# Kernel tuning notes

Hardware: AMD Instinct MI355X
Metric: run time of the kernel (lower is better)

## Reference

```python
import jax, jax.numpy as jnp
import numpy as np

M = 500000   # num_type_node_G1 (nodes in sub-graph G1_sub1)
D = 128      # embedding_dim
S = 0        # start_idx
E = 8000000  # number of nonzero adjacency entries (avg degree 16)


def setup_inputs() -> dict:
    key = jax.random.key(0)
    k1, k2 = jax.random.split(key)
    return {
        "all_node_embedding": jax.random.normal(k1, (S + M, D), dtype=jnp.float32),
        "adj_rows": jax.random.randint(k2, (E,), 0, M, dtype=jnp.int32),
    }


def reference(all_node_embedding, adj_rows):
    # emb: [M, D] sub-block of node embeddings
    emb = all_node_embedding[S:]
    # The original builds G1_sub1_three_dim_node [M, M, D] with column i equal to
    # emb[i]; its sum over axis 1 is simply the total over all sub-block nodes,
    # broadcast to every row.
    total = emb.sum(axis=0)  # [D]
    new = emb + total        # [M, D] : node_embedding + three_dim.sum(1)
    # degree per row from nonzero adjacency rows; sum_arr = 1 + degree
    deg = jax.ops.segment_sum(
        jnp.ones(adj_rows.shape, dtype=emb.dtype), adj_rows, num_segments=M
    )
    sum_arr = (1.0 + deg)[:, None]  # [M, 1]
    # new * (I - three_dim.sum(1) / sum_arr)
    new2 = new * (1.0 - total / sum_arr)  # [M, D]
    return all_node_embedding.at[S:].set(new2)
```

## Files before the change

kernel.cpp:

```cpp
#include <hip/hip_runtime.h>

#define M_ROWS   500000
#define D_COLS   128
#define E_EDGES  8000000
#define NGROUPS  (M_ROWS / 8)
#define NPBLK    2048

#define NR     16
#define BINS   (M_ROWS / NR)
#define WORDS  (BINS / 2)
#define RPB    32
#define NHB    (NR * RPB)
#define I4PS   (E_EDGES / RPB / 4)
#define MW     (M_ROWS / 2)


__global__ __launch_bounds__(256) void hist_degree_kernel(const int* __restrict__ rows,
                                                          unsigned int* __restrict__ copies) {
    __shared__ unsigned int h[WORDS];
    const int t = threadIdx.x;
    const int r = blockIdx.x & (NR - 1);
    const int s = blockIdx.x >> 4;
    for (int w = t; w < WORDS; w += 256) h[w] = 0u;
    __syncthreads();
    const unsigned int base = (unsigned int)(r * BINS);
    const int4* r4 = (const int4*)rows;
    const int i0 = s * I4PS;
    for (int i = i0 + t; i < i0 + I4PS; i += 256) {
        const int4 v = r4[i];
        unsigned int a;
        a = (unsigned int)v.x - base; if (a < BINS) atomicAdd(&h[a >> 1], (a & 1) ? 0x10000u : 1u);
        a = (unsigned int)v.y - base; if (a < BINS) atomicAdd(&h[a >> 1], (a & 1) ? 0x10000u : 1u);
        a = (unsigned int)v.z - base; if (a < BINS) atomicAdd(&h[a >> 1], (a & 1) ? 0x10000u : 1u);
        a = (unsigned int)v.w - base; if (a < BINS) atomicAdd(&h[a >> 1], (a & 1) ? 0x10000u : 1u);
    }
    __syncthreads();
    unsigned int* dst = copies + (size_t)s * MW + (size_t)r * WORDS;
    for (int w = t; w < WORDS; w += 256) dst[w] = h[w];
}

__global__ __launch_bounds__(256) void reduce_deg_kernel(const unsigned int* __restrict__ copies,
                                                         int* __restrict__ deg) {
    const int w = blockIdx.x * 256 + threadIdx.x;
    if (w >= MW) return;
    unsigned int lo = 0, hi = 0;
    #pragma unroll
    for (int s = 0; s < RPB; ++s) {
        const unsigned int v = copies[(size_t)s * MW + w];
        lo += v & 0xFFFFu;
        hi += v >> 16;
    }
    ((int2*)deg)[w] = make_int2((int)lo, (int)hi);
}

__global__ __launch_bounds__(256) void colsum_partial_kernel(const float* __restrict__ emb,
                                                             float* __restrict__ partials) {
    const int t = threadIdx.x;
    const int col4 = t & 31;
    const int sub  = t >> 5;
    float4 acc = make_float4(0.f, 0.f, 0.f, 0.f);
    for (int g = blockIdx.x; g < NGROUPS; g += gridDim.x) {
        const long row = (long)g * 8 + sub;
        const float4 v = ((const float4*)(emb + row * D_COLS))[col4];
        acc.x += v.x; acc.y += v.y; acc.z += v.z; acc.w += v.w;
    }
    __shared__ float4 red[256];
    red[t] = acc;
    __syncthreads();
    if (sub == 0) {
        float4 s = red[col4];
        #pragma unroll
        for (int j = 1; j < 8; ++j) {
            const float4 v = red[j * 32 + col4];
            s.x += v.x; s.y += v.y; s.z += v.z; s.w += v.w;
        }
        partials[(col4 * 4 + 0) * NPBLK + blockIdx.x] = s.x;
        partials[(col4 * 4 + 1) * NPBLK + blockIdx.x] = s.y;
        partials[(col4 * 4 + 2) * NPBLK + blockIdx.x] = s.z;
        partials[(col4 * 4 + 3) * NPBLK + blockIdx.x] = s.w;
    }
}

__global__ __launch_bounds__(256) void colsum_final_kernel(const float* __restrict__ partials,
                                                           float* __restrict__ total) {
    const int col = blockIdx.x;
    const int t = threadIdx.x;
    float s = 0.f;
    #pragma unroll
    for (int k = 0; k < NPBLK / 256; ++k)
        s += partials[col * NPBLK + k * 256 + t];
    __shared__ float red[256];
    red[t] = s;
    __syncthreads();
    for (int off = 128; off > 0; off >>= 1) {
        if (t < off) red[t] += red[t + off];
        __syncthreads();
    }
    if (t == 0) total[col] = red[0];
}

__global__ __launch_bounds__(256) void update_kernel(const float* __restrict__ emb,
                                                     const float* __restrict__ total,
                                                     const int* __restrict__ deg,
                                                     float* __restrict__ out) {
    __shared__ float4 t4s[32];
    const int t = threadIdx.x;
    if (t < 32) t4s[t] = ((const float4*)total)[t];
    __syncthreads();
    const int col4 = t & 31;
    const int sub  = t >> 5;
    const float4 tt = t4s[col4];
    for (int g = blockIdx.x; g < NGROUPS; g += gridDim.x) {
        const long row = (long)g * 8 + sub;
        const float invd = 1.0f / (1.0f + (float)deg[row]);
        const float4 v = ((const float4*)(emb + row * D_COLS))[col4];
        float4 o;
        o.x = (v.x + tt.x) * (1.0f - tt.x * invd);
        o.y = (v.y + tt.y) * (1.0f - tt.y * invd);
        o.z = (v.z + tt.z) * (1.0f - tt.z * invd);
        o.w = (v.w + tt.w) * (1.0f - tt.w * invd);
        ((float4*)(out + row * D_COLS))[col4] = o;
    }
}

extern "C" void kernel_launch(void* const* d_in, const int* in_sizes, int n_in,
                              void* d_out, int out_size, void* d_ws, size_t ws_size,
                              hipStream_t stream) {
    const float* emb  = (const float*)d_in[0];
    const int*   rows = (const int*)d_in[1];
    float* out      = (float*)d_out;
    float* partials = (float*)d_out;
    unsigned int* copies = (unsigned int*)((char*)d_out + (size_t)NPBLK * D_COLS * sizeof(float));
    int*   deg      = (int*)d_ws;
    float* total    = (float*)((char*)d_ws + M_ROWS * sizeof(int));

    hist_degree_kernel<<<NHB, 256, 0, stream>>>(rows, copies);
    reduce_deg_kernel<<<(MW + 255) / 256, 256, 0, stream>>>(copies, deg);
    colsum_partial_kernel<<<NPBLK, 256, 0, stream>>>(emb, partials);
    colsum_final_kernel<<<D_COLS, 256, 0, stream>>>(partials, total);
    update_kernel<<<4096, 256, 0, stream>>>(emb, total, deg, out);
}
```

Before: 635.3 us.

## Prefetch next iteration loads, enlarge histogram blocks, remap block-to-slice order

Adds one-iteration-ahead register prefetching to the histogram, column-sum and update loops so global loads overlap the atomics and arithmetic. The histogram kernel now uses 512 threads and power-of-two bin ranges (32768 bins per range), and blocks are remapped so neighbouring blocks read different input slices. The copies buffer is sized to 16 full ranges, more than M, so the reduce kernel reads a padded layout. The prefetching costs extra registers, and the larger shared histogram may reduce occupancy.

```diff
diff --git a/kernel.cpp b/kernel.cpp
--- a/kernel.cpp
+++ b/kernel.cpp
@@ -6,51 +6,61 @@
 #define NGROUPS  (M_ROWS / 8)
 #define NPBLK    2048
 
-#define NR     16
-#define BINS   (M_ROWS / NR)
-#define WORDS  (BINS / 2)
-#define RPB    32
-#define NHB    (NR * RPB)
-#define I4PS   (E_EDGES / RPB / 4)
-#define MW     (M_ROWS / 2)
+#define NR       16
+#define RBITS    15
+#define BINS     (1 << RBITS)
+#define HWORDS   (BINS / 2)
+#define RPB      32
+#define NHB      (NR * RPB)
+#define HTHR     512
+#define I4PS     (E_EDGES / RPB / 4)
+#define SLICEW   (NR * HWORDS)
+#define MW       (M_ROWS / 2)
 
 
-__global__ __launch_bounds__(256) void hist_degree_kernel(const int* __restrict__ rows,
-                                                          unsigned int* __restrict__ copies) {
-    __shared__ unsigned int h[WORDS];
-    const int t = threadIdx.x;
-    const int r = blockIdx.x & (NR - 1);
-    const int s = blockIdx.x >> 4;
-    for (int w = t; w < WORDS; w += 256) h[w] = 0u;
+__global__ __launch_bounds__(HTHR) void hist_degree_kernel(const int* __restrict__ rows,
+                                                           unsigned int* __restrict__ copies) {
+    __shared__ unsigned int h[HWORDS];
+    const int t  = threadIdx.x;
+    const int x  = blockIdx.x & 7;
+    const int g2 = blockIdx.x >> 3;
+    const int s  = x * 4 + (g2 & 3);
+    const int r  = g2 >> 2;
+    for (int w = t; w < HWORDS; w += HTHR) h[w] = 0u;
     __syncthreads();
-    const unsigned int base = (unsigned int)(r * BINS);
+    const unsigned int base = (unsigned int)r << RBITS;
     const int4* r4 = (const int4*)rows;
-    const int i0 = s * I4PS;
-    for (int i = i0 + t; i < i0 + I4PS; i += 256) {
-        const int4 v = r4[i];
+    const int iend = (s + 1) * I4PS;
+    int i = s * I4PS + t;
+    int4 v = (i < iend) ? r4[i] : make_int4(-1, -1, -1, -1);
+    while (i < iend) {
+        const int inext = i + HTHR;
+        int4 vn = make_int4(-1, -1, -1, -1);
+        if (inext < iend) vn = r4[inext];
         unsigned int a;
         a = (unsigned int)v.x - base; if (a < BINS) atomicAdd(&h[a >> 1], (a & 1) ? 0x10000u : 1u);
         a = (unsigned int)v.y - base; if (a < BINS) atomicAdd(&h[a >> 1], (a & 1) ? 0x10000u : 1u);
         a = (unsigned int)v.z - base; if (a < BINS) atomicAdd(&h[a >> 1], (a & 1) ? 0x10000u : 1u);
         a = (unsigned int)v.w - base; if (a < BINS) atomicAdd(&h[a >> 1], (a & 1) ? 0x10000u : 1u);
+        v = vn; i = inext;
     }
     __syncthreads();
-    unsigned int* dst = copies + (size_t)s * MW + (size_t)r * WORDS;
-    for (int w = t; w < WORDS; w += 256) dst[w] = h[w];
+    unsigned int* dst = copies + (size_t)s * SLICEW + (size_t)r * HWORDS;
+    for (int w = t; w < HWORDS; w += HTHR) dst[w] = h[w];
 }
 
 __global__ __launch_bounds__(256) void reduce_deg_kernel(const unsigned int* __restrict__ copies,
                                                          int* __restrict__ deg) {
-    const int w = blockIdx.x * 256 + threadIdx.x;
-    if (w >= MW) return;
+    const int w2 = blockIdx.x * 256 + threadIdx.x;
+    if (w2 >= MW) return;
     unsigned int lo = 0, hi = 0;
     #pragma unroll
     for (int s = 0; s < RPB; ++s) {
-        const unsigned int v = copies[(size_t)s * MW + w];
+        const unsigned int v = copies[(size_t)s * SLICEW + w2];
         lo += v & 0xFFFFu;
         hi += v >> 16;
     }
-    ((int2*)deg)[w] = make_int2((int)lo, (int)hi);
+    ((int2*)deg)[w2] = make_int2((int)lo, (int)hi);
 }
 
 __global__ __launch_bounds__(256) void colsum_partial_kernel(const float* __restrict__ emb,
@@ -59,10 +69,16 @@
     const int col4 = t & 31;
     const int sub  = t >> 5;
     float4 acc = make_float4(0.f, 0.f, 0.f, 0.f);
-    for (int g = blockIdx.x; g < NGROUPS; g += gridDim.x) {
-        const long row = (long)g * 8 + sub;
-        const float4 v = ((const float4*)(emb + row * D_COLS))[col4];
+    int g = blockIdx.x;
+    float4 v = ((const float4*)(emb + ((long)g * 8 + sub) * D_COLS))[col4];
+    while (true) {
+        const int gn = g + NPBLK;
+        const bool more = gn < NGROUPS;
+        float4 vn = v;
+        if (more) vn = ((const float4*)(emb + ((long)gn * 8 + sub) * D_COLS))[col4];
         acc.x += v.x; acc.y += v.y; acc.z += v.z; acc.w += v.w;
+        if (!more) break;
+        v = vn; g = gn;
     }
     __shared__ float4 red[256];
     red[t] = acc;
@@ -71,8 +87,8 @@
         float4 s = red[col4];
         #pragma unroll
         for (int j = 1; j < 8; ++j) {
-            const float4 v = red[j * 32 + col4];
-            s.x += v.x; s.y += v.y; s.z += v.z; s.w += v.w;
+            const float4 w = red[j * 32 + col4];
+            s.x += w.x; s.y += w.y; s.z += w.z; s.w += w.w;
         }
         partials[(col4 * 4 + 0) * NPBLK + blockIdx.x] = s.x;
         partials[(col4 * 4 + 1) * NPBLK + blockIdx.x] = s.y;
@@ -110,16 +126,28 @@
     const int col4 = t & 31;
     const int sub  = t >> 5;
     const float4 tt = t4s[col4];
-    for (int g = blockIdx.x; g < NGROUPS; g += gridDim.x) {
-        const long row = (long)g * 8 + sub;
-        const float invd = 1.0f / (1.0f + (float)deg[row]);
-        const float4 v = ((const float4*)(emb + row * D_COLS))[col4];
+    int g = blockIdx.x;
+    long row = (long)g * 8 + sub;
+    int d = deg[row];
+    float4 v = ((const float4*)(emb + row * D_COLS))[col4];
+    while (true) {
+        const int gn = g + (int)gridDim.x;
+        const bool more = gn < NGROUPS;
+        const long rown = (long)gn * 8 + sub;
+        int dn = d; float4 vn = v;
+        if (more) {
+            dn = deg[rown];
+            vn = ((const float4*)(emb + rown * D_COLS))[col4];
+        }
+        const float invd = 1.0f / (1.0f + (float)d);
         float4 o;
         o.x = (v.x + tt.x) * (1.0f - tt.x * invd);
         o.y = (v.y + tt.y) * (1.0f - tt.y * invd);
         o.z = (v.z + tt.z) * (1.0f - tt.z * invd);
         o.w = (v.w + tt.w) * (1.0f - tt.w * invd);
         ((float4*)(out + row * D_COLS))[col4] = o;
+        if (!more) break;
+        d = dn; v = vn; row = rown; g = gn;
     }
 }
 
@@ -134,7 +162,7 @@
     int*   deg      = (int*)d_ws;
     float* total    = (float*)((char*)d_ws + M_ROWS * sizeof(int));
 
-    hist_degree_kernel<<<NHB, 256, 0, stream>>>(rows, copies);
+    hist_degree_kernel<<<NHB, HTHR, 0, stream>>>(rows, copies);
     reduce_deg_kernel<<<(MW + 255) / 256, 256, 0, stream>>>(copies, deg);
     colsum_partial_kernel<<<NPBLK, 256, 0, stream>>>(emb, partials);
     colsum_final_kernel<<<D_COLS, 256, 0, stream>>>(partials, total);
```

After: 570.8 us. 10.2% less time.
